# Kernel optimization log

Hardware: AMD Instinct MI355X
Metric: run time of the kernel (lower is better)

The kernel has to match this reference:

```python
import jax, jax.numpy as jnp
import numpy as np

B, C, M, T = 2, 512, 16, 128
H = 8
D = C // H  # 64, divisible by 4 for 2D RoPE
G = C // 4  # GroupNorm groups = 128
S = M * T


def group_norm(x, scale, bias, groups=G, eps=1e-5):
    b, c, m, t = x.shape
    xg = x.reshape(b, groups, c // groups, m, t)
    mu = xg.mean(axis=(2, 3, 4), keepdims=True)
    var = xg.var(axis=(2, 3, 4), keepdims=True)
    xn = ((xg - mu) * jax.lax.rsqrt(var + eps)).reshape(b, c, m, t)
    return xn * scale[None, :, None, None] + bias[None, :, None, None]


def dwsep_conv(x, dw, pw):
    # depthwise 3x3 (groups=C) then pointwise 1x1
    y = jax.lax.conv_general_dilated(
        x, dw, window_strides=(1, 1), padding='SAME',
        dimension_numbers=('NCHW', 'HWIO', 'NCHW'), feature_group_count=x.shape[1])
    return jnp.einsum('bcmt,cd->bdmt', y, pw)


def rope2d(x):
    # x: [B,H,M,T,D]; first D/2 dims rotated by freq index m, last D/2 by time index t
    d = x.shape[-1]
    dh = d // 2
    q = dh // 2
    inv = 1.0 / (10000.0 ** (jnp.arange(q, dtype=jnp.float32) / q))

    def rot(v, ang):
        h = v.shape[-1] // 2
        v1, v2 = v[..., :h], v[..., h:]
        c, s = jnp.cos(ang), jnp.sin(ang)
        return jnp.concatenate([v1 * c - v2 * s, v1 * s + v2 * c], axis=-1)

    ang_f = jnp.arange(x.shape[2], dtype=jnp.float32)[:, None] * inv  # [M,q]
    ang_t = jnp.arange(x.shape[3], dtype=jnp.float32)[:, None] * inv  # [T,q]
    xf = rot(x[..., :dh], ang_f[:, None, :])  # broadcast over T
    xt = rot(x[..., dh:], ang_t)
    return jnp.concatenate([xf, xt], axis=-1)


def setup_inputs() -> dict:
    key = jax.random.key(0)
    ks = jax.random.split(key, 14)
    s = 0.02
    return {
        'x': jax.random.normal(ks[0], (B, C, M, T), jnp.float32),
        'lengths': jax.random.randint(ks[1], (B,), T // 2, T + 1),
        'gn_scale': jnp.ones((C,), jnp.float32),
        'gn_bias': jnp.zeros((C,), jnp.float32),
        'dw_q': jax.random.normal(ks[2], (3, 3, 1, C), jnp.float32) * s,
        'dw_k': jax.random.normal(ks[3], (3, 3, 1, C), jnp.float32) * s,
        'dw_v': jax.random.normal(ks[4], (3, 3, 1, C), jnp.float32) * s,
        'pw_q': jax.random.normal(ks[5], (C, C), jnp.float32) * s,
        'pw_k': jax.random.normal(ks[6], (C, C), jnp.float32) * s,
        'pw_v': jax.random.normal(ks[7], (C, C), jnp.float32) * s,
        'attn_w': jax.random.normal(ks[8], (C, C), jnp.float32) * s,
        'attn_b': jnp.zeros((C,), jnp.float32),
        'out_w': jax.random.normal(ks[9], (C, C), jnp.float32) * s,
        'out_b': jnp.zeros((C,), jnp.float32),
    }


def reference(x, lengths, gn_scale, gn_bias, dw_q, dw_k, dw_v, pw_q, pw_k, pw_v,
              attn_w, attn_b, out_w, out_b):
    residual = x
    xn = group_norm(x, gn_scale, gn_bias)

    def to_heads(y):  # [B,C,M,T] -> [B,H,M,T,D]
        return y.reshape(B, H, D, M, T).transpose(0, 1, 3, 4, 2)

    q = rope2d(to_heads(dwsep_conv(xn, dw_q, pw_q)))
    k = rope2d(to_heads(dwsep_conv(xn, dw_k, pw_k)))
    v = to_heads(dwsep_conv(xn, dw_v, pw_v))

    q = q.reshape(B, H, S, D)
    k = k.reshape(B, H, S, D)
    v = v.reshape(B, H, S, D)

    scores = jnp.einsum('bhsd,bhkd->bhsk', q, k) / np.sqrt(D).astype(np.float32)
    valid_t = jnp.arange(T)[None, :] < lengths[:, None]        # [B,T]
    valid = jnp.tile(valid_t, (1, M))                          # [B,S], token idx = m*T + t
    scores = jnp.where(valid[:, None, None, :], scores, jnp.float32(-1e9))
    attn = jax.nn.softmax(scores, axis=-1)
    o = jnp.einsum('bhsk,bhkd->bhsd', attn, v)                 # [B,H,S,D]

    o = o.transpose(0, 2, 1, 3).reshape(B, S, C)
    o = o @ attn_w + attn_b                                    # block output proj
    o = o.reshape(B, M, T, C).transpose(0, 3, 1, 2)            # [B,C,M,T]
    out = jnp.einsum('bcmt,cd->bdmt', o, out_w) + out_b[None, :, None, None]
    return residual + out
```

## Files before the change

### kernel.cpp

```cpp
#include <hip/hip_runtime.h>
#include <math.h>

#define CCH 512
#define SSQ 2048
#define MTOT 4096

typedef __bf16 bf16;
typedef __bf16 bf16x8 __attribute__((ext_vector_type(8)));
typedef __bf16 bf16x4 __attribute__((ext_vector_type(4)));
typedef float  f32x4  __attribute__((ext_vector_type(4)));

#define AS1 __attribute__((address_space(1)))
#define AS3 __attribute__((address_space(3)))
__device__ __forceinline__ void glds16(const void* g, void* l) {
    __builtin_amdgcn_global_load_lds((const AS1 void*)g, (AS3 void*)l, 16, 0, 0);
}
__device__ __forceinline__ float fexp2(float x) {
    float r; asm("v_exp_f32 %0, %1" : "=v"(r) : "v"(x)); return r;
}

__global__ __launch_bounds__(256) void gnw_kernel(const float* __restrict__ x,
        float* __restrict__ mu, float* __restrict__ rstd,
        const float* __restrict__ w0, const float* __restrict__ w1,
        const float* __restrict__ w2, const float* __restrict__ w3,
        const float* __restrict__ w4, bf16* __restrict__ wT,
        const float* __restrict__ attnb, const float* __restrict__ outb,
        float* __restrict__ bcv, float2* __restrict__ rtab) {
    __shared__ float smem[64*65];
    int tid = threadIdx.x;
    if (blockIdx.x < 256) {
        float* s_sum = smem;
        float* s_sq  = smem + 256;
        int bg = blockIdx.x;
        long base = (long)bg * 8192;
        float sum = 0.f, sq = 0.f;
#pragma unroll
        for (int r = 0; r < 32; ++r) {
            float v = x[base + r*256 + tid];
            sum += v; sq += v*v;
        }
        s_sum[tid] = sum; s_sq[tid] = sq;
        __syncthreads();
        for (int off = 128; off > 0; off >>= 1) {
            if (tid < off) { s_sum[tid] += s_sum[tid+off]; s_sq[tid] += s_sq[tid+off]; }
            __syncthreads();
        }
        if (tid == 0) {
            float m = s_sum[0] * (1.f/8192.f);
            float v = s_sq[0]  * (1.f/8192.f) - m*m;
            mu[bg] = m;
            rstd[bg] = rsqrtf(v + 1e-5f);
        }
    } else if (blockIdx.x < 576) {
        int bid = blockIdx.x - 256;
        int z = bid >> 6, r2 = bid & 63;
        int k0 = (r2 >> 3)*64, n0 = (r2 & 7)*64;
        const float* srcs[5] = {w0, w1, w2, w3, w4};
        const float* W = srcs[z];
        bf16* D = wT + (long)z * (CCH*CCH);
        float (*t)[65] = (float(*)[65])smem;
        int cI = tid & 63, r4 = tid >> 6;
#pragma unroll
        for (int p = 0; p < 16; ++p) {
            int kr = p*4 + r4;
            t[kr][cI] = W[(long)(k0+kr)*CCH + n0 + cI];
        }
        __syncthreads();
#pragma unroll
        for (int p = 0; p < 16; ++p) {
            int nr = p*4 + r4;
            D[(long)(n0+nr)*CCH + k0 + cI] = (bf16)t[cI][nr];
        }
    } else if (blockIdx.x < 608) {
        int n0 = (blockIdx.x - 576) * 16;
        float part[16];
#pragma unroll
        for (int i = 0; i < 16; ++i) part[i] = 0.f;
#pragma unroll
        for (int jj = 0; jj < 2; ++jj) {
            int j = tid*2 + jj;
            float a = attnb[j];
            const float* wr = w4 + (long)j*CCH + n0;
#pragma unroll
            for (int p = 0; p < 4; ++p) {
                float4 v4 = *(const float4*)(wr + p*4);
                part[p*4+0] += a*v4.x; part[p*4+1] += a*v4.y;
                part[p*4+2] += a*v4.z; part[p*4+3] += a*v4.w;
            }
        }
        float (*red)[16] = (float(*)[16])smem;
#pragma unroll
        for (int i = 0; i < 16; ++i) red[tid][i] = part[i];
        __syncthreads();
        for (int off = 128; off > 0; off >>= 1) {
            if (tid < off)
#pragma unroll
                for (int i = 0; i < 16; ++i) red[tid][i] += red[tid+off][i];
            __syncthreads();
        }
        if (tid < 16) bcv[n0 + tid] = red[0][tid] + outb[n0 + tid];
    } else if (blockIdx.x < 672) {
        bf16* wAc = wT + (long)5*CCH*CCH;
        int base = (blockIdx.x - 608)*4096 + tid;
#pragma unroll
        for (int p = 0; p < 16; ++p)
            wAc[base + p*256] = (bf16)w3[base + p*256];
    } else {
        int idx = (blockIdx.x - 672)*256 + tid;
        if (idx < 2304) {
            int j = (idx < 256) ? idx : idx - 256;
            int pos = j >> 4, c = j & 15;
            float invf = __expf(-(float)c * 0.5756462732485114f);
            float sn, cs;
            __sincosf((float)pos * invf, &sn, &cs);
            rtab[idx].x = cs;
            rtab[idx].y = sn;
        }
    }
}

__global__ void tn_kernel(const float* __restrict__ x, const float* __restrict__ mu,
                          const float* __restrict__ rstd, const float* __restrict__ gsc,
                          const float* __restrict__ gbs, bf16* __restrict__ xnT) {
    __shared__ float t[64][65];
    int s0 = blockIdx.x*64, c0 = blockIdx.y*64, b = blockIdx.z;
    int tid = threadIdx.x;
    int cI = tid & 63, r4 = tid >> 6;
#pragma unroll
    for (int p = 0; p < 16; ++p) {
        int cr = p*4 + r4;
        t[cr][cI] = x[((long)(b*CCH + c0 + cr))*SSQ + s0 + cI];
    }
    __syncthreads();
#pragma unroll
    for (int p = 0; p < 16; ++p) {
        int sr = p*4 + r4;
        int c = c0 + cI;
        int g = b*128 + (c >> 2);
        float v = (t[cI][sr] - mu[g]) * rstd[g] * gsc[c] + gbs[c];
        xnT[((long)(b*SSQ + s0 + sr))*CCH + c] = (bf16)v;
    }
}

__global__ __launch_bounds__(256) void dw3_kernel(const bf16* __restrict__ xnT,
        const float* __restrict__ dwq, const float* __restrict__ dwk,
        const float* __restrict__ dwv,
        bf16* __restrict__ yq, bf16* __restrict__ yk, bf16* __restrict__ yv) {
    int tid = threadIdx.x;
    int cc = (tid & 63) * 8;
    int s  = blockIdx.x*4 + (tid >> 6);
    int sl = s & (SSQ-1);
    int b  = s >> 11;
    int m = sl >> 7, t = sl & 127;
    float aq[8] = {}, ak[8] = {}, av[8] = {};
#pragma unroll
    for (int di = 0; di < 3; ++di) {
        int m2 = m + di - 1;
        if ((unsigned)m2 >= 16u) continue;
#pragma unroll
        for (int dj = 0; dj < 3; ++dj) {
            int t2 = t + dj - 1;
            if ((unsigned)t2 >= 128u) continue;
            bf16x8 xv = *(const bf16x8*)(xnT + ((long)(b*SSQ + m2*128 + t2))*CCH + cc);
            int wi = (di*3 + dj)*CCH + cc;
            float wq[8], wk[8], wv[8];
            *(float4*)&wq[0] = *(const float4*)(dwq + wi);
            *(float4*)&wq[4] = *(const float4*)(dwq + wi + 4);
            *(float4*)&wk[0] = *(const float4*)(dwk + wi);
            *(float4*)&wk[4] = *(const float4*)(dwk + wi + 4);
            *(float4*)&wv[0] = *(const float4*)(dwv + wi);
            *(float4*)&wv[4] = *(const float4*)(dwv + wi + 4);
#pragma unroll
            for (int i = 0; i < 8; ++i) {
                float xf = (float)xv[i];
                aq[i] += xf * wq[i];
                ak[i] += xf * wk[i];
                av[i] += xf * wv[i];
            }
        }
    }
    bf16x8 oq, ok, ov;
#pragma unroll
    for (int i = 0; i < 8; ++i) { oq[i] = (bf16)aq[i]; ok[i] = (bf16)ak[i]; ov[i] = (bf16)av[i]; }
    long o = (long)s*CCH + cc;
    *(bf16x8*)(yq + o) = oq;
    *(bf16x8*)(yk + o) = ok;
    *(bf16x8*)(yv + o) = ov;
}

template<int NFR>
__device__ __forceinline__ void gemm_core128(const bf16* __restrict__ A,
        const bf16* __restrict__ Wt, int m0, int n0,
        bf16* As, bf16* Bs, f32x4 (&acc)[4][NFR]) {
    int tid = threadIdx.x, lane = tid & 63, wid = tid >> 6;
    int sw = wid & 1, nw = wid >> 1;
    int col = lane & 15, quad = lane >> 4;
    const char* gA[4]; char* ldsA[4];
#pragma unroll
    for (int p = 0; p < 4; ++p) {
        int ci = tid + p*256;
        int row = ci >> 3;
        int c = (ci & 7) ^ (row & 7);
        gA[p] = (const char*)A + ((long)(m0+row)*CCH + c*8)*2;
        ldsA[p] = (char*)As + ci*16;
    }
    const char* gB[NFR]; char* ldsB[NFR];
#pragma unroll
    for (int p = 0; p < NFR; ++p) {
        int ci = tid + p*256;
        int row = ci >> 3;
        int c = (ci & 7) ^ (row & 7);
        gB[p] = (const char*)Wt + ((long)(n0+row)*CCH + c*8)*2;
        ldsB[p] = (char*)Bs + ci*16;
    }
    int rowA = sw*64 + col;
    int rowB = nw*(NFR*16) + col;
    for (int k0 = 0; k0 < CCH; k0 += 64) {
        __syncthreads();
#pragma unroll
        for (int p = 0; p < 4; ++p)   glds16(gA[p] + k0*2, ldsA[p]);
#pragma unroll
        for (int p = 0; p < NFR; ++p) glds16(gB[p] + k0*2, ldsB[p]);
        __syncthreads();
        bf16x8 af[4][2], bfr[NFR][2];
#pragma unroll
        for (int mt = 0; mt < 4; ++mt) {
            int r = rowA + mt*16;
#pragma unroll
            for (int ks = 0; ks < 2; ++ks) {
                int c = (ks*4 + quad) ^ (r & 7);
                af[mt][ks] = *(const bf16x8*)((char*)As + r*128 + c*16);
            }
        }
#pragma unroll
        for (int nt = 0; nt < NFR; ++nt) {
            int r = rowB + nt*16;
#pragma unroll
            for (int ks = 0; ks < 2; ++ks) {
                int c = (ks*4 + quad) ^ (r & 7);
                bfr[nt][ks] = *(const bf16x8*)((char*)Bs + r*128 + c*16);
            }
        }
#pragma unroll
        for (int ks = 0; ks < 2; ++ks)
#pragma unroll
            for (int mt = 0; mt < 4; ++mt)
#pragma unroll
                for (int nt = 0; nt < NFR; ++nt)
                    acc[mt][nt] = __builtin_amdgcn_mfma_f32_16x16x32_bf16(
                        af[mt][ks], bfr[nt][ks], acc[mt][nt], 0,0,0);
    }
}

__global__ __launch_bounds__(256) void gemm_qkv(const bf16* __restrict__ Abase,
        bf16* __restrict__ wT, const float2* __restrict__ rtab,
        bf16* __restrict__ qout, bf16* __restrict__ kout, bf16* __restrict__ vout) {
    __shared__ bf16 As[128*64];
    __shared__ bf16 Bs[128*64];
    int z = blockIdx.z;
    if (z == 3 && blockIdx.x >= 4) return;
    int m0 = blockIdx.x*128, n0 = blockIdx.y*128;
    const bf16* Aop = (z < 3) ? Abase + (long)z*MTOT*CCH : wT + (long)4*CCH*CCH;
    const bf16* Wop = (z < 3) ? wT + (long)z*CCH*CCH   : wT + (long)5*CCH*CCH;
    f32x4 acc[4][4] = {};
    gemm_core128<4>(Aop, Wop, m0, n0, As, Bs, acc);
    int tid = threadIdx.x, lane = tid & 63, wid = tid >> 6;
    int sw = wid & 1, nw = wid >> 1;
    int col = lane & 15, quad = lane >> 4;
    int nbase = n0 + nw*64;
    int mb = m0 + sw*64;
    if (z == 3) {
        bf16* wCt = wT + (long)6*CCH*CCH;
#pragma unroll
        for (int nt = 0; nt < 4; ++nt) {
            int n = nbase + nt*16 + col;
#pragma unroll
            for (int mt = 0; mt < 4; ++mt)
#pragma unroll
                for (int r = 0; r < 4; ++r)
                    wCt[(long)(mb + mt*16 + quad*4 + r)*CCH + n] = (bf16)acc[mt][nt][r];
        }
    } else if (z < 2) {
        bf16* outp = z ? kout : qout;
        const float sc = z ? 1.0f : 0.18033688f;
        const float2* t0 = rtab + col;
        const float2* t1 = rtab + 256 + col;
#pragma unroll
        for (int mt = 0; mt < 4; ++mt)
#pragma unroll
            for (int r = 0; r < 4; ++r) {
                int row = mb + mt*16 + quad*4 + r;
                int sl = row & (SSQ-1);
                float2 cf = t0[(sl >> 7) * 16];
                float2 ct = t1[(sl & 127) * 16];
#pragma unroll
                for (int half = 0; half < 2; ++half) {
                    float csv = half ? ct.x : cf.x;
                    float snv = half ? ct.y : cf.y;
                    float x1 = acc[mt][half*2+0][r], x2 = acc[mt][half*2+1][r];
                    outp[(long)row*CCH + nbase + half*32 + col]      = (bf16)((x1*csv - x2*snv)*sc);
                    outp[(long)row*CCH + nbase + half*32 + 16 + col] = (bf16)((x1*snv + x2*csv)*sc);
                }
            }
    } else {
#pragma unroll
        for (int mt = 0; mt < 4; ++mt)
#pragma unroll
            for (int nt = 0; nt < 4; ++nt) {
                int n = nbase + nt*16 + col;
                int row0 = mb + mt*16 + quad*4;
                int bq = row0 >> 11, sl0 = row0 & (SSQ-1);
                int sub16 = (sl0 >> 4) & 1;
                long slp = (long)(sl0 & ~31) + quad*8 + sub16*4;
                bf16x4 pk;
#pragma unroll
                for (int r = 0; r < 4; ++r) pk[r] = (bf16)acc[mt][nt][r];
                *(bf16x4*)(vout + ((long)(bq*CCH + n))*SSQ + slp) = pk;
            }
    }
}

__global__ __launch_bounds__(256) void gemm_out(const bf16* __restrict__ A,
        const bf16* __restrict__ Wt, const float* __restrict__ bias,
        const float* __restrict__ resid, float* __restrict__ outp) {
    __shared__ bf16 As[128*64];
    __shared__ bf16 Bs[64*64];
    int m0 = blockIdx.x*128, n0 = blockIdx.y*64;
    f32x4 acc[4][2] = {};
    gemm_core128<2>(A, Wt, m0, n0, As, Bs, acc);
    int tid = threadIdx.x, lane = tid & 63, wid = tid >> 6;
    int sw = wid & 1, nw = wid >> 1;
    int col = lane & 15, quad = lane >> 4;
    int nb = n0 + nw*32, mb = m0 + sw*64;
#pragma unroll
    for (int mt = 0; mt < 4; ++mt)
#pragma unroll
        for (int nt = 0; nt < 2; ++nt) {
            int n = nb + nt*16 + col;
            float bv = bias[n];
            int row0 = mb + mt*16 + quad*4;
            int b = row0 >> 11, sl0 = row0 & (SSQ-1);
            long off = ((long)(b*CCH + n))*SSQ + sl0;
            float4 rr = *(const float4*)(resid + off);
            float4 o4;
            o4.x = acc[mt][nt][0] + bv + rr.x;
            o4.y = acc[mt][nt][1] + bv + rr.y;
            o4.z = acc[mt][nt][2] + bv + rr.z;
            o4.w = acc[mt][nt][3] + bv + rr.w;
            *(float4*)(outp + off) = o4;
        }
}

__global__ __launch_bounds__(256, 2) void attn_kernel(
        const bf16* __restrict__ qb, const bf16* __restrict__ kb,
        const bf16* __restrict__ vb, const int* __restrict__ lengths,
        bf16* __restrict__ o) {
    __shared__ char KVs[2][32768];
    __shared__ float Lsm[4][4][16];
    int bid = blockIdx.x;
    int bh = bid & 15, qtb = bid >> 4;
    int b = bh >> 3, h = bh & 7;
    int tid = threadIdx.x, wid = tid >> 6, lane = tid & 63;
    int col = lane & 15, quad = lane >> 4;
    int q0 = qtb*64;
    int lenb = lengths[b];
    int thr = lenb - wid*32 - quad*4;

    const char* gK[4]; const char* gV[4];
#pragma unroll
    for (int j = 0; j < 4; ++j) {
        int s = j*64 + lane;
        int rl = s >> 3;
        int cin = s & 7;
        int csrc = cin ^ (rl & 7);
        gK[j] = (const char*)kb + ((long)(b*SSQ + wid*32 + rl))*1024 + h*128 + csrc*16;
        gV[j] = (const char*)vb + ((long)(b*CCH + h*64 + j*16 + col))*4096 + (wid*4 + quad)*16;
    }
    char* ldsK = (char*)KVs + wid*4096 + lane*16;
    char* ldsV = (char*)KVs + 16384 + wid*4096 + lane*16;

    const bf16* qp = qb + (long)(b*SSQ)*CCH + h*64;
    bf16x8 qf[4][2];
#pragma unroll
    for (int qt = 0; qt < 4; ++qt)
#pragma unroll
        for (int dc = 0; dc < 2; ++dc)
            qf[qt][dc] = *(const bf16x8*)(qp + (long)(q0 + qt*16 + col)*CCH + dc*32 + quad*8);

    f32x4 of[4][4] = {};
    float ls[4] = {};
    int cswz7 = col & 7;
    int kc0 = (quad ^ cswz7)*16;
    int kc1 = ((4 + quad) ^ cswz7)*16;

#pragma unroll
    for (int j = 0; j < 4; ++j) glds16(gK[j], ldsK + j*1024);
#pragma unroll
    for (int j = 0; j < 4; ++j) glds16(gV[j], ldsV + j*1024);
#pragma unroll
    for (int j = 0; j < 4; ++j) glds16(gK[j] + 131072L, ldsK + 32768 + j*1024);
#pragma unroll
    for (int j = 0; j < 4; ++j) glds16(gV[j] + 256L, ldsV + 32768 + j*1024);

    for (int t = 0; t < 16; ++t) {
        if (t == 15) { asm volatile("s_waitcnt vmcnt(0)" ::: "memory"); }
        else         { asm volatile("s_waitcnt vmcnt(8)" ::: "memory"); }
        __builtin_amdgcn_sched_barrier(0);
        const char* K = KVs[t & 1] + wid*4096;
        const char* V = KVs[t & 1] + 16384 + wid*4096;
        bf16x8 kf[2][2], vf[4];
#pragma unroll
        for (int sub = 0; sub < 2; ++sub) {
            kf[sub][0] = *(const bf16x8*)(K + sub*2048 + col*128 + kc0);
            kf[sub][1] = *(const bf16x8*)(K + sub*2048 + col*128 + kc1);
        }
#pragma unroll
        for (int dt = 0; dt < 4; ++dt)
            vf[dt] = *(const bf16x8*)(V + dt*1024 + lane*16);
        asm volatile("s_waitcnt lgkmcnt(0)" ::: "memory");
        __builtin_amdgcn_sched_barrier(0);
        if (t < 14) {
            int bsel = (t & 1)*32768;
#pragma unroll
            for (int j = 0; j < 4; ++j) glds16(gK[j] + (long)(t+2)*131072, ldsK + bsel + j*1024);
#pragma unroll
            for (int j = 0; j < 4; ++j) glds16(gV[j] + (long)(t+2)*256,    ldsV + bsel + j*1024);
        }
        __builtin_amdgcn_sched_barrier(0);
        f32x4 sc[2][4];
#pragma unroll
        for (int sub = 0; sub < 2; ++sub) {
            f32x4 m;
#pragma unroll
            for (int r = 0; r < 4; ++r) m[r] = (sub*16 + r < thr) ? 0.f : -10000.f;
#pragma unroll
            for (int qt = 0; qt < 4; ++qt) sc[sub][qt] = m;
        }
        __builtin_amdgcn_s_setprio(1);
#pragma unroll
        for (int sub = 0; sub < 2; ++sub)
#pragma unroll
            for (int qt = 0; qt < 4; ++qt) {
                sc[sub][qt] = __builtin_amdgcn_mfma_f32_16x16x32_bf16(kf[sub][0], qf[qt][0], sc[sub][qt], 0,0,0);
                sc[sub][qt] = __builtin_amdgcn_mfma_f32_16x16x32_bf16(kf[sub][1], qf[qt][1], sc[sub][qt], 0,0,0);
            }
        __builtin_amdgcn_s_setprio(0);
        bf16x8 pf[4];
#pragma unroll
        for (int qt = 0; qt < 4; ++qt) {
            float s = 0.f;
#pragma unroll
            for (int r = 0; r < 4; ++r) {
                float e0 = fexp2(sc[0][qt][r]);
                float e1 = fexp2(sc[1][qt][r]);
                pf[qt][r]     = (bf16)e0;
                pf[qt][4 + r] = (bf16)e1;
                s += e0 + e1;
            }
            ls[qt] += s;
        }
        __builtin_amdgcn_s_setprio(1);
#pragma unroll
        for (int dt = 0; dt < 4; ++dt)
#pragma unroll
            for (int qt = 0; qt < 4; ++qt)
                of[qt][dt] = __builtin_amdgcn_mfma_f32_16x16x32_bf16(pf[qt], vf[dt], of[qt][dt], 0,0,0);
        __builtin_amdgcn_s_setprio(0);
    }

#pragma unroll
    for (int qt = 0; qt < 4; ++qt) {
        ls[qt] += __shfl_xor(ls[qt], 16);
        ls[qt] += __shfl_xor(ls[qt], 32);
    }
    __syncthreads();
    float* Om = (float*)KVs;
#pragma unroll
    for (int qt = 0; qt < 4; ++qt)
#pragma unroll
        for (int dt = 0; dt < 4; ++dt)
#pragma unroll
            for (int r = 0; r < 4; ++r)
                Om[(wid*64 + qt*16 + quad*4 + r)*64 + dt*16 + col] = of[qt][dt][r];
    if (quad == 0)
#pragma unroll
        for (int qt = 0; qt < 4; ++qt) Lsm[wid][qt][col] = ls[qt];
    __syncthreads();
    bf16* ob = o + (long)(b*SSQ + q0)*CCH + h*64;
#pragma unroll
    for (int i = 0; i < 16; ++i) {
        int rr = wid*16 + i;
        float v = Om[rr*64 + lane] + Om[(64 + rr)*64 + lane]
                + Om[(128 + rr)*64 + lane] + Om[(192 + rr)*64 + lane];
        float l = Lsm[0][wid][i] + Lsm[1][wid][i] + Lsm[2][wid][i] + Lsm[3][wid][i];
        ob[(long)rr*CCH + lane] = (bf16)(v / l);
    }
}

extern "C" void kernel_launch(void* const* d_in, const int* in_sizes, int n_in,
                              void* d_out, int out_size, void* d_ws, size_t ws_size,
                              hipStream_t stream) {
    const float* x        = (const float*)d_in[0];
    const int*   lengths  = (const int*)  d_in[1];
    const float* gn_scale = (const float*)d_in[2];
    const float* gn_bias  = (const float*)d_in[3];
    const float* dw_q     = (const float*)d_in[4];
    const float* dw_k     = (const float*)d_in[5];
    const float* dw_v     = (const float*)d_in[6];
    const float* pw_q     = (const float*)d_in[7];
    const float* pw_k     = (const float*)d_in[8];
    const float* pw_v     = (const float*)d_in[9];
    const float* attn_w   = (const float*)d_in[10];
    const float* attn_b   = (const float*)d_in[11];
    const float* out_w    = (const float*)d_in[12];
    const float* out_b    = (const float*)d_in[13];
    float* out = (float*)d_out;

    char* w = (char*)d_ws;
    float* mu   = (float*)w;
    float* rstd = (float*)(w + 1024);
    float* bcv  = (float*)(w + 2048);
    bf16* wT    = (bf16*)(w + 4096);
    bf16* wCt = wT + (long)6*CCH*CCH;
    float2* rtab = (float2*)(w + 0x00390000);
    bf16* xnT  = (bf16*)(w + 0x00400000);
    bf16* yT   = (bf16*)(w + 0x00800000);
    bf16* qbf  = (bf16*)(w + 0x01400000);
    bf16* kbf  = (bf16*)(w + 0x01800000);
    bf16* vbf  = (bf16*)(w + 0x01C00000);
    bf16* obf  = (bf16*)(w + 0x02000000);

    gnw_kernel<<<681, 256, 0, stream>>>(x, mu, rstd, pw_q, pw_k, pw_v, attn_w, out_w,
                                        wT, attn_b, out_b, bcv, rtab);
    tn_kernel<<<dim3(32,8,2), 256, 0, stream>>>(x, mu, rstd, gn_scale, gn_bias, xnT);
    dw3_kernel<<<MTOT/4, 256, 0, stream>>>(xnT, dw_q, dw_k, dw_v,
                                           yT, yT + (long)MTOT*CCH, yT + (long)2*MTOT*CCH);

    gemm_qkv<<<dim3(MTOT/128, CCH/128, 4), 256, 0, stream>>>(yT, wT, rtab, qbf, kbf, vbf);

    attn_kernel<<<512, 256, 0, stream>>>(qbf, kbf, vbf, lengths, obf);

    gemm_out<<<dim3(MTOT/128, CCH/64), 256, 0, stream>>>(obf, wCt, bcv, x, out);
}
```

Measured before the change: 155.1 us.

## Load V fragments directly to registers, halve LDS, raise attention occupancy

```diff
diff --git a/kernel.cpp b/kernel.cpp
--- a/kernel.cpp
+++ b/kernel.cpp
@@ -351,11 +351,79 @@
         }
 }
 
-__global__ __launch_bounds__(256, 2) void attn_kernel(
+__device__ __forceinline__ void attn_tile13(int t, const char* ldsKr, char* ldsK,
+        const char* const (&gK)[4], const char* const (&gV)[4],
+        const bf16x8 (&qf)[4][2], int thr, int col, int quad, int kc0, int kc1,
+        bf16x8 (&vCur)[4], bf16x8 (&vNxt)[4], f32x4 (&of)[4][4], float (&ls)[4]) {
+    if (t == 15) { asm volatile("s_waitcnt vmcnt(4)" ::: "memory"); }
+    else         { asm volatile("s_waitcnt vmcnt(8)" ::: "memory"); }
+    __builtin_amdgcn_sched_barrier(0);
+    const char* K = ldsKr + (t & 1)*16384;
+    bf16x8 kf[2][2];
+#pragma unroll
+    for (int sub = 0; sub < 2; ++sub) {
+        kf[sub][0] = *(const bf16x8*)(K + sub*2048 + col*128 + kc0);
+        kf[sub][1] = *(const bf16x8*)(K + sub*2048 + col*128 + kc1);
+    }
+    asm volatile("s_waitcnt lgkmcnt(0)" ::: "memory");
+    __builtin_amdgcn_sched_barrier(0);
+    if (t < 14) {
+#pragma unroll
+        for (int j = 0; j < 4; ++j)
+            glds16(gK[j] + (long)(t+2)*131072, ldsK + (t & 1)*16384 + j*1024);
+    }
+    if (t < 15) {
+#pragma unroll
+        for (int j = 0; j < 4; ++j)
+            vNxt[j] = *(const bf16x8*)(gV[j] + (long)(t+1)*256);
+    }
+    __builtin_amdgcn_sched_barrier(0);
+    f32x4 sc[2][4];
+#pragma unroll
+    for (int sub = 0; sub < 2; ++sub) {
+        f32x4 m;
+#pragma unroll
+        for (int r = 0; r < 4; ++r) m[r] = (sub*16 + r < thr) ? 0.f : -10000.f;
+#pragma unroll
+        for (int qt = 0; qt < 4; ++qt) sc[sub][qt] = m;
+    }
+    __builtin_amdgcn_s_setprio(1);
+#pragma unroll
+    for (int sub = 0; sub < 2; ++sub)
+#pragma unroll
+        for (int qt = 0; qt < 4; ++qt) {
+            sc[sub][qt] = __builtin_amdgcn_mfma_f32_16x16x32_bf16(kf[sub][0], qf[qt][0], sc[sub][qt], 0,0,0);
+            sc[sub][qt] = __builtin_amdgcn_mfma_f32_16x16x32_bf16(kf[sub][1], qf[qt][1], sc[sub][qt], 0,0,0);
+        }
+    __builtin_amdgcn_s_setprio(0);
+    bf16x8 pf[4];
+#pragma unroll
+    for (int qt = 0; qt < 4; ++qt) {
+        float s = 0.f;
+#pragma unroll
+        for (int r = 0; r < 4; ++r) {
+            float e0 = fexp2(sc[0][qt][r]);
+            float e1 = fexp2(sc[1][qt][r]);
+            pf[qt][r]     = (bf16)e0;
+            pf[qt][4 + r] = (bf16)e1;
+            s += e0 + e1;
+        }
+        ls[qt] += s;
+    }
+    __builtin_amdgcn_s_setprio(1);
+#pragma unroll
+    for (int dt = 0; dt < 4; ++dt)
+#pragma unroll
+        for (int qt = 0; qt < 4; ++qt)
+            of[qt][dt] = __builtin_amdgcn_mfma_f32_16x16x32_bf16(pf[qt], vCur[dt], of[qt][dt], 0,0,0);
+    __builtin_amdgcn_s_setprio(0);
+}
+
+__global__ __launch_bounds__(256, 3) void attn_kernel(
         const bf16* __restrict__ qb, const bf16* __restrict__ kb,
         const bf16* __restrict__ vb, const int* __restrict__ lengths,
         bf16* __restrict__ o) {
-    __shared__ char KVs[2][32768];
+    __shared__ char Ks[2][16384];
     __shared__ float Lsm[4][4][16];
     int bid = blockIdx.x;
     int bh = bid & 15, qtb = bid >> 4;
@@ -376,8 +444,8 @@
         gK[j] = (const char*)kb + ((long)(b*SSQ + wid*32 + rl))*1024 + h*128 + csrc*16;
         gV[j] = (const char*)vb + ((long)(b*CCH + h*64 + j*16 + col))*4096 + (wid*4 + quad)*16;
     }
-    char* ldsK = (char*)KVs + wid*4096 + lane*16;
-    char* ldsV = (char*)KVs + 16384 + wid*4096 + lane*16;
+    char* ldsK = (char*)Ks + wid*4096 + lane*16;
+    const char* ldsKr = (const char*)Ks + wid*4096;
 
     const bf16* qp = qb + (long)(b*SSQ)*CCH + h*64;
     bf16x8 qf[4][2];
@@ -393,79 +461,17 @@
     int kc0 = (quad ^ cswz7)*16;
     int kc1 = ((4 + quad) ^ cswz7)*16;
 
+    bf16x8 vA[4], vB[4];
 #pragma unroll
     for (int j = 0; j < 4; ++j) glds16(gK[j], ldsK + j*1024);
 #pragma unroll
-    for (int j = 0; j < 4; ++j) glds16(gV[j], ldsV + j*1024);
-#pragma unroll
-    for (int j = 0; j < 4; ++j) glds16(gK[j] + 131072L, ldsK + 32768 + j*1024);
-#pragma unroll
-    for (int j = 0; j < 4; ++j) glds16(gV[j] + 256L, ldsV + 32768 + j*1024);
-
-    for (int t = 0; t < 16; ++t) {
-        if (t == 15) { asm volatile("s_waitcnt vmcnt(0)" ::: "memory"); }
-        else         { asm volatile("s_waitcnt vmcnt(8)" ::: "memory"); }
-        __builtin_amdgcn_sched_barrier(0);
-        const char* K = KVs[t & 1] + wid*4096;
-        const char* V = KVs[t & 1] + 16384 + wid*4096;
-        bf16x8 kf[2][2], vf[4];
-#pragma unroll
-        for (int sub = 0; sub < 2; ++sub) {
-            kf[sub][0] = *(const bf16x8*)(K + sub*2048 + col*128 + kc0);
-            kf[sub][1] = *(const bf16x8*)(K + sub*2048 + col*128 + kc1);
-        }
-#pragma unroll
-        for (int dt = 0; dt < 4; ++dt)
-            vf[dt] = *(const bf16x8*)(V + dt*1024 + lane*16);
-        asm volatile("s_waitcnt lgkmcnt(0)" ::: "memory");
-        __builtin_amdgcn_sched_barrier(0);
-        if (t < 14) {
-            int bsel = (t & 1)*32768;
-#pragma unroll
-            for (int j = 0; j < 4; ++j) glds16(gK[j] + (long)(t+2)*131072, ldsK + bsel + j*1024);
-#pragma unroll
-            for (int j = 0; j < 4; ++j) glds16(gV[j] + (long)(t+2)*256,    ldsV + bsel + j*1024);
-        }
-        __builtin_amdgcn_sched_barrier(0);
-        f32x4 sc[2][4];
-#pragma unroll
-        for (int sub = 0; sub < 2; ++sub) {
-            f32x4 m;
-#pragma unroll
-            for (int r = 0; r < 4; ++r) m[r] = (sub*16 + r < thr) ? 0.f : -10000.f;
-#pragma unroll
-            for (int qt = 0; qt < 4; ++qt) sc[sub][qt] = m;
-        }
-        __builtin_amdgcn_s_setprio(1);
-#pragma unroll
-        for (int sub = 0; sub < 2; ++sub)
-#pragma unroll
-            for (int qt = 0; qt < 4; ++qt) {
-                sc[sub][qt] = __builtin_amdgcn_mfma_f32_16x16x32_bf16(kf[sub][0], qf[qt][0], sc[sub][qt], 0,0,0);
-                sc[sub][qt] = __builtin_amdgcn_mfma_f32_16x16x32_bf16(kf[sub][1], qf[qt][1], sc[sub][qt], 0,0,0);
-            }
-        __builtin_amdgcn_s_setprio(0);
-        bf16x8 pf[4];
-#pragma unroll
-        for (int qt = 0; qt < 4; ++qt) {
-            float s = 0.f;
-#pragma unroll
-            for (int r = 0; r < 4; ++r) {
-                float e0 = fexp2(sc[0][qt][r]);
-                float e1 = fexp2(sc[1][qt][r]);
-                pf[qt][r]     = (bf16)e0;
-                pf[qt][4 + r] = (bf16)e1;
-                s += e0 + e1;
-            }
-            ls[qt] += s;
-        }
-        __builtin_amdgcn_s_setprio(1);
-#pragma unroll
-        for (int dt = 0; dt < 4; ++dt)
-#pragma unroll
-            for (int qt = 0; qt < 4; ++qt)
-                of[qt][dt] = __builtin_amdgcn_mfma_f32_16x16x32_bf16(pf[qt], vf[dt], of[qt][dt], 0,0,0);
-        __builtin_amdgcn_s_setprio(0);
+    for (int j = 0; j < 4; ++j) glds16(gK[j] + 131072L, ldsK + 16384 + j*1024);
+#pragma unroll
+    for (int j = 0; j < 4; ++j) vA[j] = *(const bf16x8*)(gV[j]);
+
+    for (int t2 = 0; t2 < 16; t2 += 2) {
+        attn_tile13(t2,     ldsKr, ldsK, gK, gV, qf, thr, col, quad, kc0, kc1, vA, vB, of, ls);
+        attn_tile13(t2 + 1, ldsKr, ldsK, gK, gV, qf, thr, col, quad, kc0, kc1, vB, vA, of, ls);
     }
 
 #pragma unroll
@@ -474,26 +480,32 @@
         ls[qt] += __shfl_xor(ls[qt], 32);
     }
     __syncthreads();
-    float* Om = (float*)KVs;
-#pragma unroll
-    for (int qt = 0; qt < 4; ++qt)
-#pragma unroll
-        for (int dt = 0; dt < 4; ++dt)
-#pragma unroll
-            for (int r = 0; r < 4; ++r)
-                Om[(wid*64 + qt*16 + quad*4 + r)*64 + dt*16 + col] = of[qt][dt][r];
-    if (quad == 0)
-#pragma unroll
-        for (int qt = 0; qt < 4; ++qt) Lsm[wid][qt][col] = ls[qt];
-    __syncthreads();
+    float* Om = (float*)Ks;
     bf16* ob = o + (long)(b*SSQ + q0)*CCH + h*64;
-#pragma unroll
-    for (int i = 0; i < 16; ++i) {
-        int rr = wid*16 + i;
-        float v = Om[rr*64 + lane] + Om[(64 + rr)*64 + lane]
-                + Om[(128 + rr)*64 + lane] + Om[(192 + rr)*64 + lane];
-        float l = Lsm[0][wid][i] + Lsm[1][wid][i] + Lsm[2][wid][i] + Lsm[3][wid][i];
-        ob[(long)rr*CCH + lane] = (bf16)(v / l);
+    int dl = lane & 31, rh = lane >> 5;
+#pragma unroll
+    for (int p = 0; p < 2; ++p) {
+        if (p) __syncthreads();
+#pragma unroll
+        for (int qt = 0; qt < 4; ++qt)
+#pragma unroll
+            for (int dtl = 0; dtl < 2; ++dtl)
+#pragma unroll
+                for (int r = 0; r < 4; ++r)
+                    Om[(wid*64 + qt*16 + quad*4 + r)*32 + dtl*16 + col] = of[qt][p*2 + dtl][r];
+        if (p == 0 && quad == 0)
+#pragma unroll
+            for (int qt = 0; qt < 4; ++qt) Lsm[wid][qt][col] = ls[qt];
+        __syncthreads();
+#pragma unroll
+        for (int it = 0; it < 8; ++it) {
+            int rr = wid*16 + it*2 + rh;
+            float v = Om[rr*32 + dl] + Om[(64 + rr)*32 + dl]
+                    + Om[(128 + rr)*32 + dl] + Om[(192 + rr)*32 + dl];
+            float l = Lsm[0][rr>>4][rr&15] + Lsm[1][rr>>4][rr&15]
+                    + Lsm[2][rr>>4][rr&15] + Lsm[3][rr>>4][rr&15];
+            ob[(long)rr*CCH + p*32 + dl] = (bf16)(v / l);
+        }
     }
 }
 
```

After: 211.3 us. 36.2% more time.
